# Optimization experiments

Hardware: AMD Instinct MI355X
Metric: run time of the kernel (lower is better)

## Reference

```python
import jax, jax.numpy as jnp
import numpy as np

N_NODES = 50000
N_EDGES = 600000
IN_DIM = 128
HID = 256
OUT = 3


def setup_inputs() -> dict:
    key = jax.random.key(0)
    ks = jax.random.split(key, 10)
    x = jax.random.normal(ks[0], (N_NODES, IN_DIM), dtype=jnp.float32)
    edge_index = jax.random.randint(ks[1], (2, N_EDGES), 0, N_NODES, dtype=jnp.int64)
    s = lambda k, shp: jax.random.normal(k, shp, dtype=jnp.float32) * (1.0 / np.sqrt(shp[0]))
    return {
        "x": x,
        "edge_index": edge_index,
        # SAGEConv1: lin_l (applied to aggregated neighbors, with bias), lin_r (root, no bias)
        "W1l": s(ks[2], (IN_DIM, HID)), "b1": jnp.zeros((HID,), jnp.float32), "W1r": s(ks[3], (IN_DIM, HID)),
        # SAGEConv2
        "W2l": s(ks[4], (HID, HID)), "b2": jnp.zeros((HID,), jnp.float32), "W2r": s(ks[5], (HID, HID)),
        # classification head
        "Wh": s(ks[6], (HID, OUT)), "bh": jnp.zeros((OUT,), jnp.float32),
    }


def _sage_conv(x, edge_index, Wl, b, Wr):
    """PyG SAGEConv with mean aggregation: out = lin_l(mean_{j->i} x_j) + lin_r(x_i)."""
    src, dst = edge_index[0], edge_index[1]
    n = x.shape[0]
    # gather source features and scatter-mean onto targets
    msg_sum = jax.ops.segment_sum(x[src], dst, num_segments=n)          # [N, d]
    deg = jax.ops.segment_sum(jnp.ones((src.shape[0],), x.dtype), dst, num_segments=n)
    mean = msg_sum / jnp.maximum(deg, 1.0)[:, None]                      # isolated nodes -> 0
    return mean @ Wl + b + x @ Wr


def reference(x, edge_index, W1l, b1, W1r, W2l, b2, W2r, Wh, bh):
    h = jax.nn.relu(_sage_conv(x, edge_index, W1l, b1, W1r))
    # dropout(p=0.2) is identity in eval mode
    h = jax.nn.relu(_sage_conv(h, edge_index, W2l, b2, W2r))
    return h @ Wh + bh
```

## Files before the change

kernel.cpp:

```cpp
#include <hip/hip_runtime.h>
#include <hip/hip_bf16.h>

#define N_NODES 50000
#define N_EDGES 600000
#define IN_DIM 128
#define HID 256
#define OUT_DIM 3

#define M_PAD 50048

#define SCAN_B 256
#define SCAN_NB ((N_NODES + SCAN_B - 1) / SCAN_B)

typedef __bf16 bf16x8 __attribute__((ext_vector_type(8)));
typedef float f32x4 __attribute__((ext_vector_type(4)));

static __device__ __forceinline__ unsigned short f2b(float f) {
    union { float f; unsigned u; } u; u.f = f;
    unsigned r = u.u + 0x7fffu + ((u.u >> 16) & 1u);
    return (unsigned short)(r >> 16);
}
static __device__ __forceinline__ float b2f(unsigned short b) {
    union { unsigned u; float f; } u; u.u = ((unsigned)b) << 16;
    return u.f;
}


__global__ void count_deg_kernel(const int* __restrict__ dst, int* __restrict__ counts) {
    int e = blockIdx.x * blockDim.x + threadIdx.x;
    if (e < N_EDGES) atomicAdd(&counts[dst[e]], 1);
}

__global__ __launch_bounds__(256) void block_sum_kernel(const int* __restrict__ counts,
                                                        int* __restrict__ partial) {
    int node = blockIdx.x * SCAN_B + threadIdx.x;
    int v = (node < N_NODES) ? counts[node] : 0;
#pragma unroll
    for (int off = 32; off > 0; off >>= 1) v += __shfl_down(v, off);
    __shared__ int ws[4];
    if ((threadIdx.x & 63) == 0) ws[threadIdx.x >> 6] = v;
    __syncthreads();
    if (threadIdx.x == 0) partial[blockIdx.x] = ws[0] + ws[1] + ws[2] + ws[3];
}

__global__ __launch_bounds__(256) void scan_partial_kernel(int* __restrict__ partial) {
    __shared__ int s[SCAN_B];
    int t = threadIdx.x;
    int v = (t < SCAN_NB) ? partial[t] : 0;
    s[t] = v;
    __syncthreads();
    for (int off = 1; off < SCAN_B; off <<= 1) {
        int u = (t >= off) ? s[t - off] : 0;
        __syncthreads();
        s[t] += u;
        __syncthreads();
    }
    if (t < SCAN_NB) partial[t] = s[t] - v;
}

__global__ __launch_bounds__(256) void write_rowptr_kernel(const int* __restrict__ counts,
                                                           const int* __restrict__ partial,
                                                           int* __restrict__ row_ptr) {
    __shared__ int s[SCAN_B];
    int t = threadIdx.x;
    int node = blockIdx.x * SCAN_B + t;
    int v = (node < N_NODES) ? counts[node] : 0;
    s[t] = v;
    __syncthreads();
    for (int off = 1; off < SCAN_B; off <<= 1) {
        int u = (t >= off) ? s[t - off] : 0;
        __syncthreads();
        s[t] += u;
        __syncthreads();
    }
    if (node < N_NODES) row_ptr[node] = partial[blockIdx.x] + s[t] - v;
    if (node == 0) row_ptr[N_NODES] = N_EDGES;
}

__global__ void fill_csr_kernel(const int* __restrict__ src, const int* __restrict__ dst,
                                const int* __restrict__ row_ptr, int* __restrict__ cursor,
                                int* __restrict__ csr_src) {
    int e = blockIdx.x * blockDim.x + threadIdx.x;
    if (e < N_EDGES) {
        int d = dst[e];
        int pos = atomicAdd(&cursor[d], 1);
        csr_src[row_ptr[d] + pos] = src[e];
    }
}


__global__ void cast_f2b_kernel(const float* __restrict__ in, unsigned short* __restrict__ out, int n) {
    int i = blockIdx.x * blockDim.x + threadIdx.x;
    if (i * 4 < n) {
        float4 v = ((const float4*)in)[i];
        ushort4 o;
        o.x = f2b(v.x); o.y = f2b(v.y); o.z = f2b(v.z); o.w = f2b(v.w);
        ((ushort4*)out)[i] = o;
    }
}

__global__ void tcast4_kernel(const float* __restrict__ W1l, const float* __restrict__ W1r,
                              const float* __restrict__ W2l, const float* __restrict__ W2r,
                              unsigned short* __restrict__ W1lt, unsigned short* __restrict__ W1rt,
                              unsigned short* __restrict__ W2lt, unsigned short* __restrict__ W2rt) {
    int i = blockIdx.x * blockDim.x + threadIdx.x;
    const float* in; unsigned short* out; int K, base;
    if (i < 32768)        { in = W1l; out = W1lt; K = IN_DIM; base = 0; }
    else if (i < 65536)   { in = W1r; out = W1rt; K = IN_DIM; base = 32768; }
    else if (i < 131072)  { in = W2l; out = W2lt; K = HID;    base = 65536; }
    else if (i < 196608)  { in = W2r; out = W2rt; K = HID;    base = 131072; }
    else return;
    int j = i - base;
    int k = j >> 8;
    int n = j & 255;
    out[(size_t)n * K + k] = f2b(in[j]);
}

__global__ void init_out_kernel(const float* __restrict__ bh, float* __restrict__ out) {
    int i = blockIdx.x * blockDim.x + threadIdx.x;
    if (i < N_NODES * 3) out[i] = bh[i % 3];
}


static __device__ __forceinline__ void addv(float* acc, uint4 v) {
    acc[0] += b2f((unsigned short)(v.x & 0xffff));
    acc[1] += b2f((unsigned short)(v.x >> 16));
    acc[2] += b2f((unsigned short)(v.y & 0xffff));
    acc[3] += b2f((unsigned short)(v.y >> 16));
    acc[4] += b2f((unsigned short)(v.z & 0xffff));
    acc[5] += b2f((unsigned short)(v.z >> 16));
    acc[6] += b2f((unsigned short)(v.w & 0xffff));
    acc[7] += b2f((unsigned short)(v.w >> 16));
}

static __device__ __forceinline__ uint4 pack8(const float* a) {
    uint4 pk;
    pk.x = (unsigned)f2b(a[0]) | ((unsigned)f2b(a[1]) << 16);
    pk.y = (unsigned)f2b(a[2]) | ((unsigned)f2b(a[3]) << 16);
    pk.z = (unsigned)f2b(a[4]) | ((unsigned)f2b(a[5]) << 16);
    pk.w = (unsigned)f2b(a[6]) | ((unsigned)f2b(a[7]) << 16);
    return pk;
}

__global__ __launch_bounds__(256) void agg_mean256_kernel(const unsigned short* __restrict__ feat,
                                                          const int* __restrict__ row_ptr,
                                                          const int* __restrict__ csr_src,
                                                          unsigned short* __restrict__ out) {
    int node = blockIdx.x * 4 + (threadIdx.x >> 6);
    if (node >= N_NODES) return;
    int lane = threadIdx.x & 63;
    int half = lane >> 5, lh = lane & 31;
    const uint4* f4 = (const uint4*)feat;
    float acc[8];
#pragma unroll
    for (int j = 0; j < 8; j++) acc[j] = 0.f;
    int beg = row_ptr[node], end = row_ptr[node + 1];
    int i = beg;
    for (; i + 4 <= end; i += 4) {
        int sA = csr_src[i + half];
        int sB = csr_src[i + 2 + half];
        uint4 vA = f4[(size_t)sA * 32 + lh];
        uint4 vB = f4[(size_t)sB * 32 + lh];
        addv(acc, vA);
        addv(acc, vB);
    }
    if (i + 2 <= end) {
        int s = csr_src[i + half];
        addv(acc, f4[(size_t)s * 32 + lh]);
        i += 2;
    }
    if (i < end && half == 0) {
        int s = csr_src[i];
        addv(acc, f4[(size_t)s * 32 + lh]);
    }
    float inv = (end > beg) ? 1.0f / (float)(end - beg) : 0.0f;
#pragma unroll
    for (int j = 0; j < 8; j++) {
        acc[j] += __shfl_xor(acc[j], 32);
        acc[j] *= inv;
    }
    if (half == 0) ((uint4*)(out + (size_t)node * 256))[lh] = pack8(acc);
}

__global__ __launch_bounds__(256) void agg_mean128_kernel(const unsigned short* __restrict__ feat,
                                                          const int* __restrict__ row_ptr,
                                                          const int* __restrict__ csr_src,
                                                          unsigned short* __restrict__ out) {
    int node = blockIdx.x * 4 + (threadIdx.x >> 6);
    if (node >= N_NODES) return;
    int lane = threadIdx.x & 63;
    int q = lane >> 4, lq = lane & 15;
    const uint4* f4 = (const uint4*)feat;
    float acc[8];
#pragma unroll
    for (int j = 0; j < 8; j++) acc[j] = 0.f;
    int beg = row_ptr[node], end = row_ptr[node + 1];
    int i = beg;
    for (; i + 8 <= end; i += 8) {
        int sA = csr_src[i + q];
        int sB = csr_src[i + 4 + q];
        uint4 vA = f4[(size_t)sA * 16 + lq];
        uint4 vB = f4[(size_t)sB * 16 + lq];
        addv(acc, vA);
        addv(acc, vB);
    }
    if (i + 4 <= end) {
        int s = csr_src[i + q];
        addv(acc, f4[(size_t)s * 16 + lq]);
        i += 4;
    }
    int rem = end - i;
    if (q < rem) {
        int s = csr_src[i + q];
        addv(acc, f4[(size_t)s * 16 + lq]);
    }
    float inv = (end > beg) ? 1.0f / (float)(end - beg) : 0.0f;
#pragma unroll
    for (int j = 0; j < 8; j++) {
        acc[j] += __shfl_xor(acc[j], 32);
        acc[j] += __shfl_xor(acc[j], 16);
        acc[j] *= inv;
    }
    if (q == 0) ((uint4*)(out + (size_t)node * 128))[lq] = pack8(acc);
}


template <int KP>
static __device__ __forceinline__ void gemm_pipe_loop(
    const unsigned short* __restrict__ A0, const unsigned short* __restrict__ W0t,
    const unsigned short* __restrict__ A1, const unsigned short* __restrict__ W1t,
    unsigned short* As, unsigned short* Bs,
    int m0, int n0, int t, int w, int quad, int lr, f32x4 (&acc)[2][8]) {
    constexpr int KI = KP / 32;
    constexpr int NIT = 2 * KI;
    const int kb = t & 3;
    const int r  = t >> 2;

    const unsigned short* Aa[2] = {A0, A1};
    const unsigned short* Wa[2] = {W0t, W1t};

    uint4 ra0, ra1, rb0, rb1;
    auto gload = [&](int it) {
        int p = it / KI;
        int k0 = (it % KI) * 32 + kb * 8;
        const unsigned short* A = Aa[p];
        const unsigned short* Wt = Wa[p];
        ra0 = *(const uint4*)(A + (size_t)(m0 + r) * KP + k0);
        ra1 = *(const uint4*)(A + (size_t)(m0 + 64 + r) * KP + k0);
        rb0 = *(const uint4*)(Wt + (size_t)(n0 + r) * KP + k0);
        rb1 = *(const uint4*)(Wt + (size_t)(n0 + 64 + r) * KP + k0);
    };
    auto wlds = [&](int buf) {
        unsigned short* pa = As + buf * 4096;
        unsigned short* pb = Bs + buf * 4096;
        *(uint4*)&pa[(kb * 128 + r) * 8] = ra0;
        *(uint4*)&pa[(kb * 128 + 64 + r) * 8] = ra1;
        *(uint4*)&pb[(kb * 128 + r) * 8] = rb0;
        *(uint4*)&pb[(kb * 128 + 64 + r) * 8] = rb1;
    };

    gload(0);
    wlds(0);
    __syncthreads();
    for (int it = 0; it < NIT; ++it) {
        if (it + 1 < NIT) gload(it + 1);
        const unsigned short* pa = As + (it & 1) * 4096;
        const unsigned short* pb = Bs + (it & 1) * 4096;
        bf16x8 a[2], b[8];
        a[0] = *(const bf16x8*)&pa[(quad * 128 + w * 32 + lr) * 8];
        a[1] = *(const bf16x8*)&pa[(quad * 128 + w * 32 + 16 + lr) * 8];
#pragma unroll
        for (int nt = 0; nt < 8; nt++)
            b[nt] = *(const bf16x8*)&pb[(quad * 128 + nt * 16 + lr) * 8];
#pragma unroll
        for (int mt = 0; mt < 2; mt++)
#pragma unroll
            for (int nt = 0; nt < 8; nt++)
                acc[mt][nt] = __builtin_amdgcn_mfma_f32_16x16x32_bf16(a[mt], b[nt], acc[mt][nt], 0, 0, 0);
        if (it + 1 < NIT) {
            wlds((it + 1) & 1);
            __syncthreads();
        }
    }
}

template <int KP>
__global__ __launch_bounds__(256) void gemm_pipe_kernel(
    const unsigned short* __restrict__ A0, const unsigned short* __restrict__ W0t,
    const unsigned short* __restrict__ A1, const unsigned short* __restrict__ W1t,
    const float* __restrict__ bias, unsigned short* __restrict__ out, int M) {
    __shared__ __align__(16) unsigned short As[2 * 4096];
    __shared__ __align__(16) unsigned short Bs[2 * 4096];

    const int t = threadIdx.x;
    const int w = t >> 6, l = t & 63;
    const int quad = l >> 4, lr = l & 15;
    const int m0 = blockIdx.x * 128, n0 = blockIdx.y * 128;

    f32x4 acc[2][8];
    const f32x4 zero = {0.f, 0.f, 0.f, 0.f};
#pragma unroll
    for (int mt = 0; mt < 2; mt++)
#pragma unroll
        for (int nt = 0; nt < 8; nt++) acc[mt][nt] = zero;

    float bias_r[8];
#pragma unroll
    for (int nt = 0; nt < 8; nt++) bias_r[nt] = bias[n0 + nt * 16 + lr];

    gemm_pipe_loop<KP>(A0, W0t, A1, W1t, As, Bs, m0, n0, t, w, quad, lr, acc);

#pragma unroll
    for (int mt = 0; mt < 2; mt++)
#pragma unroll
        for (int r = 0; r < 4; r++) {
            int gm = m0 + w * 32 + mt * 16 + quad * 4 + r;
            if (gm >= M) continue;
            unsigned short* orow = out + (size_t)gm * HID;
#pragma unroll
            for (int nt = 0; nt < 8; nt++) {
                float v = fmaxf(acc[mt][nt][r] + bias_r[nt], 0.f);
                orow[n0 + nt * 16 + lr] = f2b(v);
            }
        }
}

template <int KP>
__global__ __launch_bounds__(256) void gemm_pipe_head_kernel(
    const unsigned short* __restrict__ A0, const unsigned short* __restrict__ W0t,
    const unsigned short* __restrict__ A1, const unsigned short* __restrict__ W1t,
    const float* __restrict__ bias, const float* __restrict__ Wh,
    float* __restrict__ out, int M) {
    __shared__ __align__(16) unsigned short As[2 * 4096];
    __shared__ __align__(16) unsigned short Bs[2 * 4096];

    const int t = threadIdx.x;
    const int w = t >> 6, l = t & 63;
    const int quad = l >> 4, lr = l & 15;
    const int m0 = blockIdx.x * 128, n0 = blockIdx.y * 128;

    f32x4 acc[2][8];
    const f32x4 zero = {0.f, 0.f, 0.f, 0.f};
#pragma unroll
    for (int mt = 0; mt < 2; mt++)
#pragma unroll
        for (int nt = 0; nt < 8; nt++) acc[mt][nt] = zero;

    float bias_r[8];
    float wh_r[8][3];
#pragma unroll
    for (int nt = 0; nt < 8; nt++) {
        int gn = n0 + nt * 16 + lr;
        bias_r[nt] = bias[gn];
        wh_r[nt][0] = Wh[gn * 3 + 0];
        wh_r[nt][1] = Wh[gn * 3 + 1];
        wh_r[nt][2] = Wh[gn * 3 + 2];
    }

    gemm_pipe_loop<KP>(A0, W0t, A1, W1t, As, Bs, m0, n0, t, w, quad, lr, acc);

#pragma unroll
    for (int mt = 0; mt < 2; mt++)
#pragma unroll
        for (int r = 0; r < 4; r++) {
            int gm = m0 + w * 32 + mt * 16 + quad * 4 + r;
            float p0 = 0.f, p1 = 0.f, p2 = 0.f;
#pragma unroll
            for (int nt = 0; nt < 8; nt++) {
                float v = fmaxf(acc[mt][nt][r] + bias_r[nt], 0.f);
                p0 += v * wh_r[nt][0];
                p1 += v * wh_r[nt][1];
                p2 += v * wh_r[nt][2];
            }
#pragma unroll
            for (int off = 1; off < 16; off <<= 1) {
                p0 += __shfl_xor(p0, off);
                p1 += __shfl_xor(p1, off);
                p2 += __shfl_xor(p2, off);
            }
            if (lr == 0 && gm < M) {
                atomicAdd(&out[(size_t)gm * 3 + 0], p0);
                atomicAdd(&out[(size_t)gm * 3 + 1], p1);
                atomicAdd(&out[(size_t)gm * 3 + 2], p2);
            }
        }
}


extern "C" void kernel_launch(void* const* d_in, const int* in_sizes, int n_in,
                              void* d_out, int out_size, void* d_ws, size_t ws_size,
                              hipStream_t stream) {
    const float* x   = (const float*)d_in[0];
    const int*   ei  = (const int*)d_in[1];
    const int*   src = ei;
    const int*   dst = ei + N_EDGES;
    const float* W1l = (const float*)d_in[2];
    const float* b1  = (const float*)d_in[3];
    const float* W1r = (const float*)d_in[4];
    const float* W2l = (const float*)d_in[5];
    const float* b2  = (const float*)d_in[6];
    const float* W2r = (const float*)d_in[7];
    const float* Wh  = (const float*)d_in[8];
    const float* bh  = (const float*)d_in[9];
    float* out = (float*)d_out;

    char* ws = (char*)d_ws;
    size_t off = 0;
    auto alloc = [&](size_t bytes) -> void* {
        void* p = ws + off;
        off = (off + bytes + 255) & ~(size_t)255;
        return p;
    };
    int* counts   = (int*)alloc((size_t)N_NODES * 4);
    int* row_ptr  = (int*)alloc((size_t)(N_NODES + 1) * 4);
    int* cursor   = (int*)alloc((size_t)N_NODES * 4);
    int* partial  = (int*)alloc((size_t)SCAN_NB * 4);
    int* csr_src  = (int*)alloc((size_t)N_EDGES * 4);
    unsigned short* xb   = (unsigned short*)alloc((size_t)M_PAD * IN_DIM * 2);
    unsigned short* agg  = (unsigned short*)alloc((size_t)M_PAD * HID * 2);
    unsigned short* h1   = (unsigned short*)alloc((size_t)M_PAD * HID * 2);
    unsigned short* W1lt = (unsigned short*)alloc((size_t)IN_DIM * HID * 2);
    unsigned short* W1rt = (unsigned short*)alloc((size_t)IN_DIM * HID * 2);
    unsigned short* W2lt = (unsigned short*)alloc((size_t)HID * HID * 2);
    unsigned short* W2rt = (unsigned short*)alloc((size_t)HID * HID * 2);

    hipMemsetAsync(counts, 0, (size_t)N_NODES * 4, stream);
    hipMemsetAsync(cursor, 0, (size_t)N_NODES * 4, stream);

    const int eblocks = (N_EDGES + 255) / 256;
    count_deg_kernel<<<eblocks, 256, 0, stream>>>(dst, counts);
    block_sum_kernel<<<SCAN_NB, SCAN_B, 0, stream>>>(counts, partial);
    scan_partial_kernel<<<1, SCAN_B, 0, stream>>>(partial);
    write_rowptr_kernel<<<SCAN_NB, SCAN_B, 0, stream>>>(counts, partial, row_ptr);
    fill_csr_kernel<<<eblocks, 256, 0, stream>>>(src, dst, row_ptr, cursor, csr_src);

    {
        int n = N_NODES * IN_DIM;
        cast_f2b_kernel<<<(n / 4 + 255) / 256, 256, 0, stream>>>(x, xb, n);
        tcast4_kernel<<<(196608 + 255) / 256, 256, 0, stream>>>(W1l, W1r, W2l, W2r,
                                                                W1lt, W1rt, W2lt, W2rt);
        init_out_kernel<<<(N_NODES * 3 + 255) / 256, 256, 0, stream>>>(bh, out);
    }

    const int nblocks4 = (N_NODES + 3) / 4;
    dim3 gg(M_PAD / 128, HID / 128);

    agg_mean128_kernel<<<nblocks4, 256, 0, stream>>>(xb, row_ptr, csr_src, agg);
    gemm_pipe_kernel<IN_DIM><<<gg, 256, 0, stream>>>(agg, W1lt, xb, W1rt, b1, h1, N_NODES);

    agg_mean256_kernel<<<nblocks4, 256, 0, stream>>>(h1, row_ptr, csr_src, agg);
    gemm_pipe_head_kernel<HID><<<gg, 256, 0, stream>>>(agg, W2lt, h1, W2rt, b2, Wh, out, N_NODES);
}
```

Measured before the change: 288.1 us.

## Fuse setup kernels into one launch and deepen gather unroll in aggregation

New measurement: 282.2 us. -2.0%, faster.

```diff
diff --git a/kernel.cpp b/kernel.cpp
--- a/kernel.cpp
+++ b/kernel.cpp
@@ -26,10 +26,44 @@
 }
 
 
-__global__ void count_deg_kernel(const int* __restrict__ dst, int* __restrict__ counts) {
-    int e = blockIdx.x * blockDim.x + threadIdx.x;
-    if (e < N_EDGES) atomicAdd(&counts[dst[e]], 1);
-}
+#define SETUP_CAST (N_NODES * IN_DIM / 4)
+#define SETUP_T1 (SETUP_CAST + 196608)
+#define SETUP_T2 (SETUP_T1 + N_NODES * 3)
+#define SETUP_TOT (SETUP_T2 + N_EDGES)
+
+__global__ __launch_bounds__(256) void setup_kernel(
+    const float* __restrict__ x, unsigned short* __restrict__ xb,
+    const float* __restrict__ W1l, const float* __restrict__ W1r,
+    const float* __restrict__ W2l, const float* __restrict__ W2r,
+    unsigned short* __restrict__ W1lt, unsigned short* __restrict__ W1rt,
+    unsigned short* __restrict__ W2lt, unsigned short* __restrict__ W2rt,
+    const float* __restrict__ bh, float* __restrict__ out,
+    const int* __restrict__ dst, int* __restrict__ counts) {
+    int i = blockIdx.x * blockDim.x + threadIdx.x;
+    if (i < SETUP_CAST) {
+        float4 v = ((const float4*)x)[i];
+        ushort4 o;
+        o.x = f2b(v.x); o.y = f2b(v.y); o.z = f2b(v.z); o.w = f2b(v.w);
+        ((ushort4*)xb)[i] = o;
+    } else if (i < SETUP_T1) {
+        int j = i - SETUP_CAST;
+        const float* in; unsigned short* ow; int K;
+        if (j < 32768)       { in = W1l; ow = W1lt; K = IN_DIM; }
+        else if (j < 65536)  { in = W1r; ow = W1rt; K = IN_DIM; j -= 32768; }
+        else if (j < 131072) { in = W2l; ow = W2lt; K = HID;    j -= 65536; }
+        else                 { in = W2r; ow = W2rt; K = HID;    j -= 131072; }
+        int k = j >> 8;
+        int n = j & 255;
+        ow[(size_t)n * K + k] = f2b(in[j]);
+    } else if (i < SETUP_T2) {
+        int j = i - SETUP_T1;
+        out[j] = bh[j % 3];
+    } else if (i < SETUP_TOT) {
+        int e = i - SETUP_T2;
+        atomicAdd(&counts[dst[e]], 1);
+    }
+}
+
 
 __global__ __launch_bounds__(256) void block_sum_kernel(const int* __restrict__ counts,
                                                         int* __restrict__ partial) {
@@ -89,39 +123,6 @@
 }
 
 
-__global__ void cast_f2b_kernel(const float* __restrict__ in, unsigned short* __restrict__ out, int n) {
-    int i = blockIdx.x * blockDim.x + threadIdx.x;
-    if (i * 4 < n) {
-        float4 v = ((const float4*)in)[i];
-        ushort4 o;
-        o.x = f2b(v.x); o.y = f2b(v.y); o.z = f2b(v.z); o.w = f2b(v.w);
-        ((ushort4*)out)[i] = o;
-    }
-}
-
-__global__ void tcast4_kernel(const float* __restrict__ W1l, const float* __restrict__ W1r,
-                              const float* __restrict__ W2l, const float* __restrict__ W2r,
-                              unsigned short* __restrict__ W1lt, unsigned short* __restrict__ W1rt,
-                              unsigned short* __restrict__ W2lt, unsigned short* __restrict__ W2rt) {
-    int i = blockIdx.x * blockDim.x + threadIdx.x;
-    const float* in; unsigned short* out; int K, base;
-    if (i < 32768)        { in = W1l; out = W1lt; K = IN_DIM; base = 0; }
-    else if (i < 65536)   { in = W1r; out = W1rt; K = IN_DIM; base = 32768; }
-    else if (i < 131072)  { in = W2l; out = W2lt; K = HID;    base = 65536; }
-    else if (i < 196608)  { in = W2r; out = W2rt; K = HID;    base = 131072; }
-    else return;
-    int j = i - base;
-    int k = j >> 8;
-    int n = j & 255;
-    out[(size_t)n * K + k] = f2b(in[j]);
-}
-
-__global__ void init_out_kernel(const float* __restrict__ bh, float* __restrict__ out) {
-    int i = blockIdx.x * blockDim.x + threadIdx.x;
-    if (i < N_NODES * 3) out[i] = bh[i % 3];
-}
-
-
 static __device__ __forceinline__ void addv(float* acc, uint4 v) {
     acc[0] += b2f((unsigned short)(v.x & 0xffff));
     acc[1] += b2f((unsigned short)(v.x >> 16));
@@ -156,23 +157,31 @@
     for (int j = 0; j < 8; j++) acc[j] = 0.f;
     int beg = row_ptr[node], end = row_ptr[node + 1];
     int i = beg;
-    for (; i + 4 <= end; i += 4) {
-        int sA = csr_src[i + half];
-        int sB = csr_src[i + 2 + half];
-        uint4 vA = f4[(size_t)sA * 32 + lh];
-        uint4 vB = f4[(size_t)sB * 32 + lh];
-        addv(acc, vA);
-        addv(acc, vB);
-    }
-    if (i + 2 <= end) {
-        int s = csr_src[i + half];
-        addv(acc, f4[(size_t)s * 32 + lh]);
-        i += 2;
-    }
-    if (i < end && half == 0) {
-        int s = csr_src[i];
-        addv(acc, f4[(size_t)s * 32 + lh]);
-    }
+    for (; i + 8 <= end; i += 8) {
+        int s0 = csr_src[i + half];
+        int s1 = csr_src[i + 2 + half];
+        int s2 = csr_src[i + 4 + half];
+        int s3 = csr_src[i + 6 + half];
+        uint4 v0 = f4[(size_t)s0 * 32 + lh];
+        uint4 v1 = f4[(size_t)s1 * 32 + lh];
+        uint4 v2 = f4[(size_t)s2 * 32 + lh];
+        uint4 v3 = f4[(size_t)s3 * 32 + lh];
+        addv(acc, v0);
+        addv(acc, v1);
+        addv(acc, v2);
+        addv(acc, v3);
+    }
+    int r = end - i;
+    uint4 u0, u1, u2, ut;
+    bool odd = (r & 1) && (half == 0);
+    if (r >= 2) { int s = csr_src[i + half];     u0 = f4[(size_t)s * 32 + lh]; }
+    if (r >= 4) { int s = csr_src[i + 2 + half]; u1 = f4[(size_t)s * 32 + lh]; }
+    if (r >= 6) { int s = csr_src[i + 4 + half]; u2 = f4[(size_t)s * 32 + lh]; }
+    if (odd)    { int s = csr_src[end - 1];      ut = f4[(size_t)s * 32 + lh]; }
+    if (r >= 2) addv(acc, u0);
+    if (r >= 4) addv(acc, u1);
+    if (r >= 6) addv(acc, u2);
+    if (odd) addv(acc, ut);
     float inv = (end > beg) ? 1.0f / (float)(end - beg) : 0.0f;
 #pragma unroll
     for (int j = 0; j < 8; j++) {
@@ -196,24 +205,33 @@
     for (int j = 0; j < 8; j++) acc[j] = 0.f;
     int beg = row_ptr[node], end = row_ptr[node + 1];
     int i = beg;
-    for (; i + 8 <= end; i += 8) {
-        int sA = csr_src[i + q];
-        int sB = csr_src[i + 4 + q];
-        uint4 vA = f4[(size_t)sA * 16 + lq];
-        uint4 vB = f4[(size_t)sB * 16 + lq];
-        addv(acc, vA);
-        addv(acc, vB);
-    }
-    if (i + 4 <= end) {
-        int s = csr_src[i + q];
-        addv(acc, f4[(size_t)s * 16 + lq]);
-        i += 4;
-    }
-    int rem = end - i;
-    if (q < rem) {
-        int s = csr_src[i + q];
-        addv(acc, f4[(size_t)s * 16 + lq]);
-    }
+    for (; i + 16 <= end; i += 16) {
+        int s0 = csr_src[i + q];
+        int s1 = csr_src[i + 4 + q];
+        int s2 = csr_src[i + 8 + q];
+        int s3 = csr_src[i + 12 + q];
+        uint4 v0 = f4[(size_t)s0 * 16 + lq];
+        uint4 v1 = f4[(size_t)s1 * 16 + lq];
+        uint4 v2 = f4[(size_t)s2 * 16 + lq];
+        uint4 v3 = f4[(size_t)s3 * 16 + lq];
+        addv(acc, v0);
+        addv(acc, v1);
+        addv(acc, v2);
+        addv(acc, v3);
+    }
+    int r = end - i;
+    int rem = r & 3;
+    int tb = i + (r & ~3);
+    bool tl = q < rem;
+    uint4 u0, u1, u2, ut;
+    if (r >= 4)  { int s = csr_src[i + q];     u0 = f4[(size_t)s * 16 + lq]; }
+    if (r >= 8)  { int s = csr_src[i + 4 + q]; u1 = f4[(size_t)s * 16 + lq]; }
+    if (r >= 12) { int s = csr_src[i + 8 + q]; u2 = f4[(size_t)s * 16 + lq]; }
+    if (tl)      { int s = csr_src[tb + q];    ut = f4[(size_t)s * 16 + lq]; }
+    if (r >= 4)  addv(acc, u0);
+    if (r >= 8)  addv(acc, u1);
+    if (r >= 12) addv(acc, u2);
+    if (tl) addv(acc, ut);
     float inv = (end > beg) ? 1.0f / (float)(end - beg) : 0.0f;
 #pragma unroll
     for (int j = 0; j < 8; j++) {
@@ -427,21 +445,15 @@
     hipMemsetAsync(counts, 0, (size_t)N_NODES * 4, stream);
     hipMemsetAsync(cursor, 0, (size_t)N_NODES * 4, stream);
 
+    setup_kernel<<<(SETUP_TOT + 255) / 256, 256, 0, stream>>>(
+        x, xb, W1l, W1r, W2l, W2r, W1lt, W1rt, W2lt, W2rt, bh, out, dst, counts);
+
     const int eblocks = (N_EDGES + 255) / 256;
-    count_deg_kernel<<<eblocks, 256, 0, stream>>>(dst, counts);
     block_sum_kernel<<<SCAN_NB, SCAN_B, 0, stream>>>(counts, partial);
     scan_partial_kernel<<<1, SCAN_B, 0, stream>>>(partial);
     write_rowptr_kernel<<<SCAN_NB, SCAN_B, 0, stream>>>(counts, partial, row_ptr);
     fill_csr_kernel<<<eblocks, 256, 0, stream>>>(src, dst, row_ptr, cursor, csr_src);
 
-    {
-        int n = N_NODES * IN_DIM;
-        cast_f2b_kernel<<<(n / 4 + 255) / 256, 256, 0, stream>>>(x, xb, n);
-        tcast4_kernel<<<(196608 + 255) / 256, 256, 0, stream>>>(W1l, W1r, W2l, W2r,
-                                                                W1lt, W1rt, W2lt, W2rt);
-        init_out_kernel<<<(N_NODES * 3 + 255) / 256, 256, 0, stream>>>(bh, out);
-    }
-
     const int nblocks4 = (N_NODES + 3) / 4;
     dim3 gg(M_PAD / 128, HID / 128);
 
```
